# Optimization experiments

Hardware: AMD Instinct MI355X
Metric: run time of the kernel (lower is better)

The kernel has to match this reference:

```python
import jax, jax.numpy as jnp
import numpy as np

MAX_OBJECTS = 20
NODE_DIM = 16
HIDDEN = 64
N_OPS = 8
N_COLORS = 10
B = 65536


def _lin(x, w, b):
    # torch nn.Linear: w is [out, in]
    return x @ w.T + b


def _ln(x, g, b, eps=1e-5):
    mu = x.mean(-1, keepdims=True)
    var = ((x - mu) ** 2).mean(-1, keepdims=True)
    return (x - mu) / jnp.sqrt(var + eps) * g + b


def setup_inputs() -> dict:
    key = jax.random.key(0)
    ks = jax.random.split(key, 32)
    s = 0.1
    d = {
        'node_feats': jax.random.normal(ks[0], (B, MAX_OBJECTS, NODE_DIM), jnp.float32),
        'n_nodes': jax.random.randint(ks[1], (B,), 1, MAX_OBJECTS + 1).astype(jnp.int32),
        'rnn_state': jax.random.normal(ks[2], (B, HIDDEN), jnp.float32),
        'prev_op_onehot': jnp.zeros((B, N_OPS), jnp.float32),
        'ne_w': jax.random.normal(ks[3], (HIDDEN, NODE_DIM)) * s,
        'ne_b': jnp.zeros((HIDDEN,)),
        'mp1_w1': jax.random.normal(ks[4], (HIDDEN, 2 * HIDDEN)) * s,
        'mp1_b1': jnp.zeros((HIDDEN,)),
        'mp1_w2': jax.random.normal(ks[5], (HIDDEN, HIDDEN)) * s,
        'mp1_b2': jnp.zeros((HIDDEN,)),
        'n1_g': jnp.ones((HIDDEN,)),
        'n1_b': jnp.zeros((HIDDEN,)),
        'mp2_w1': jax.random.normal(ks[6], (HIDDEN, 2 * HIDDEN)) * s,
        'mp2_b1': jnp.zeros((HIDDEN,)),
        'mp2_w2': jax.random.normal(ks[7], (HIDDEN, HIDDEN)) * s,
        'mp2_b2': jnp.zeros((HIDDEN,)),
        'n2_g': jnp.ones((HIDDEN,)),
        'n2_b': jnp.zeros((HIDDEN,)),
        'gru_wih': jax.random.normal(ks[8], (3 * HIDDEN, HIDDEN + N_OPS)) * s,
        'gru_whh': jax.random.normal(ks[9], (3 * HIDDEN, HIDDEN)) * s,
        'gru_bih': jnp.zeros((3 * HIDDEN,)),
        'gru_bhh': jnp.zeros((3 * HIDDEN,)),
        'op_w': jax.random.normal(ks[10], (N_OPS, HIDDEN)) * s,
        'op_b': jnp.zeros((N_OPS,)),
        'c1_w': jax.random.normal(ks[11], (N_COLORS, HIDDEN)) * s,
        'c1_b': jnp.zeros((N_COLORS,)),
        'c2_w': jax.random.normal(ks[12], (N_COLORS, HIDDEN)) * s,
        'c2_b': jnp.zeros((N_COLORS,)),
        'pq_w': jax.random.normal(ks[13], (HIDDEN, HIDDEN)) * s,
        'pq_b': jnp.zeros((HIDDEN,)),
        'pk_w': jax.random.normal(ks[14], (HIDDEN, HIDDEN)) * s,
        'pk_b': jnp.zeros((HIDDEN,)),
    }
    return d


def _forward(node_feats, n_nodes, rnn_state, prev_op_onehot,
             ne_w, ne_b, mp1_w1, mp1_b1, mp1_w2, mp1_b2, n1_g, n1_b,
             mp2_w1, mp2_b1, mp2_w2, mp2_b2, n2_g, n2_b,
             gru_wih, gru_whh, gru_bih, gru_bhh,
             op_w, op_b, c1_w, c1_b, c2_w, c2_b, pq_w, pq_b, pk_w, pk_b):
    # ---- encode_graph ----
    h = _lin(node_feats, ne_w, ne_b)                                   # [B, N, H]
    mask = jnp.arange(MAX_OBJECTS)[None, :] < n_nodes[:, None]         # [B, N]
    mf = mask.astype(h.dtype)[..., None]                               # [B, N, 1]
    cnt = jnp.clip(mf.sum(1, keepdims=True), 1.0)                      # [B, 1, 1]
    msg = (h * mf).sum(1, keepdims=True) / cnt                         # [B, 1, H]
    x1 = jnp.concatenate([h, jnp.broadcast_to(msg, h.shape)], -1)
    h = h + _lin(jax.nn.relu(_lin(x1, mp1_w1, mp1_b1)), mp1_w2, mp1_b2)
    h = _ln(h, n1_g, n1_b) * mf
    msg = (h * mf).sum(1, keepdims=True) / cnt
    x2 = jnp.concatenate([h, jnp.broadcast_to(msg, h.shape)], -1)
    h = h + _lin(jax.nn.relu(_lin(x2, mp2_w1, mp2_b1)), mp2_w2, mp2_b2)
    h = _ln(h, n2_g, n2_b) * mf
    graph_vec = (h * mf).sum(1) / jnp.clip(mf.sum(1), 1.0)             # [B, H]
    # ---- step (GRUCell + heads + pointer) ----
    x = jnp.concatenate([graph_vec, prev_op_onehot], -1)               # [B, H+n_ops]
    gi = x @ gru_wih.T + gru_bih                                       # [B, 3H]
    gh = rnn_state @ gru_whh.T + gru_bhh                               # [B, 3H]
    H = HIDDEN
    r = jax.nn.sigmoid(gi[:, :H] + gh[:, :H])
    z = jax.nn.sigmoid(gi[:, H:2 * H] + gh[:, H:2 * H])
    n = jnp.tanh(gi[:, 2 * H:] + r * gh[:, 2 * H:])
    new_state = (1.0 - z) * n + z * rnn_state                          # [B, H]
    op_logits = _lin(new_state, op_w, op_b)
    c1_logits = _lin(new_state, c1_w, c1_b)
    c2_logits = _lin(new_state, c2_w, c2_b)
    query = _lin(new_state, pq_w, pq_b)[:, None, :]                    # [B, 1, H]
    keys = _lin(h, pk_w, pk_b)                                         # [B, N, H]
    ptr_logits = (query * keys).sum(-1)                                # [B, N]
    ptr_logits = jnp.where(mask, ptr_logits, jnp.asarray(-1e9, ptr_logits.dtype))
    return op_logits, c1_logits, c2_logits, ptr_logits, new_state


def reference(node_feats, n_nodes, rnn_state, prev_op_onehot,
              ne_w, ne_b, mp1_w1, mp1_b1, mp1_w2, mp1_b2, n1_g, n1_b,
              mp2_w1, mp2_b1, mp2_w2, mp2_b2, n2_g, n2_b,
              gru_wih, gru_whh, gru_bih, gru_bhh,
              op_w, op_b, c1_w, c1_b, c2_w, c2_b, pq_w, pq_b, pk_w, pk_b):
    return _forward(node_feats, n_nodes, rnn_state, prev_op_onehot,
                    ne_w, ne_b, mp1_w1, mp1_b1, mp1_w2, mp1_b2, n1_g, n1_b,
                    mp2_w1, mp2_b1, mp2_w2, mp2_b2, n2_g, n2_b,
                    gru_wih, gru_whh, gru_bih, gru_bhh,
                    op_w, op_b, c1_w, c1_b, c2_w, c2_b, pq_w, pq_b, pk_w, pk_b)
```

## Files before the change

kernel.cpp:

```cpp
#include <hip/hip_runtime.h>
#include <hip/hip_bf16.h>
#include <cstdint>

#define NM 20
#define NBIN 20
#define MAXB 65536

typedef __attribute__((ext_vector_type(8))) short bf16x8;
typedef __attribute__((ext_vector_type(4))) float f32x4;
typedef __attribute__((ext_vector_type(4))) unsigned int u32x4;

union FU { bf16x8 h; u32x4 u; };

#define MFMA(A, Bf, C) __builtin_amdgcn_mfma_f32_16x16x32_bf16((A), (Bf), (C), 0, 0, 0)

#define F_NE    0
#define F_M1W1  2048
#define F_M1W2  10240
#define F_M2W1  14336
#define F_M2W2  22528
#define F_WIH   26624
#define F_WHH   45056
#define F_PQ    57344
#define F_PK    61440
#define F_PACK  65536
#define F_BNE   67584
#define F_B11   67648
#define F_B12   67712
#define F_G1    67776
#define F_L1    67840
#define F_B21   67904
#define F_B22   67968
#define F_G2    68032
#define F_L2    68096
#define F_TOTAL 68160

__device__ __align__(16) short g_fr[F_TOTAL];
__device__ __align__(16) float g_grb[4][64];
__device__ int g_hist[NBIN];
__device__ int g_off[NBIN];
__device__ int g_done;
__device__ int g_perm[MAXB];

__device__ __forceinline__ short bf16rn(float x) {
  unsigned u = __float_as_uint(x);
  u += 0x7fffu + ((u >> 16) & 1u);
  return (short)(u >> 16);
}
__device__ __forceinline__ float bf2f(short s) {
  return __uint_as_float(((unsigned)(unsigned short)s) << 16);
}
__device__ __forceinline__ unsigned pk2(float lo, float hi) {
  __hip_bfloat162 t = __float22bfloat162_rn(float2{lo, hi});
  return *reinterpret_cast<unsigned*>(&t);
}
__device__ __forceinline__ float fsig(float x) {
  return __builtin_amdgcn_rcpf(1.f + __expf(-x));
}
__device__ __forceinline__ float ftanh(float x) {
  return 1.f - 2.f * __builtin_amdgcn_rcpf(1.f + __expf(2.f * x));
}
__device__ __forceinline__ int s64(int r) {
  int mb = r >> 4, qq = (r >> 2) & 3, i = r & 3;
  return (mb >> 1) * 32 + qq * 8 + (mb & 1) * 4 + i;
}

#define LDF(off) (*(const bf16x8*)(g_fr + (off) + lane * 8))
#define LDB(off, c) (*(const bf16x8*)(g_fr + (off) + (c) * 32 + q * 8))
#define GAF(off) (*(const bf16x8*)(gA + (off)))
#define GBF(off, c) (*(const bf16x8*)(gB + (off) + (c) * 32))

#define BUILDA(OFS, MB, KC, ROWX, GET)                                 \
  for (int idx = t; idx < (MB) * (KC) * 512; idx += T) {               \
    int j = idx & 7, ln = (idx >> 3) & 63, f = idx >> 9;               \
    int mb = f / (KC), kc = f % (KC);                                  \
    int m = mb * 16 + (ln & 15);                                       \
    int k = kc * 32 + (ln >> 4) * 8 + j;                               \
    int row = (ROWX);                                                  \
    (void)row; (void)k; (void)m;                                       \
    g_fr[(OFS) + idx] = bf16rn(GET);                                   \
  }

__global__ void __launch_bounds__(256)
prep_frag(const float* __restrict__ ne_w,
          const float* __restrict__ m1w1, const float* __restrict__ m1w2,
          const float* __restrict__ m2w1, const float* __restrict__ m2w2,
          const float* __restrict__ wih,  const float* __restrict__ whh,
          const float* __restrict__ pqw,  const float* __restrict__ opw,
          const float* __restrict__ c1w,  const float* __restrict__ c2w,
          const float* __restrict__ pkw,
          const float* __restrict__ ne_b,
          const float* __restrict__ m1b1, const float* __restrict__ m1b2,
          const float* __restrict__ n1g,  const float* __restrict__ n1b,
          const float* __restrict__ m2b1, const float* __restrict__ m2b2,
          const float* __restrict__ n2g,  const float* __restrict__ n2b,
          const float* __restrict__ bih,  const float* __restrict__ bhh)
{
  const int t = blockIdx.x * blockDim.x + threadIdx.x;
  const int T = gridDim.x * blockDim.x;
  if (blockIdx.x == 0 && threadIdx.x < NBIN) g_hist[threadIdx.x] = 0;
  if (blockIdx.x == 0 && threadIdx.x == 0) g_done = 0;
  BUILDA(F_NE,   4, 1, s64(m), (k < 16 ? ne_w[row * 16 + k] : (k == 16 ? ne_b[row] : 0.f)))
  BUILDA(F_M1W1, 4, 4, s64(m), m1w1[row * 128 + k])
  BUILDA(F_M1W2, 4, 2, s64(m), m1w2[row * 64 + k])
  BUILDA(F_M2W1, 4, 4, s64(m), m2w1[row * 128 + k])
  BUILDA(F_M2W2, 4, 2, s64(m), m2w2[row * 64 + k])
  BUILDA(F_WIH, 12, 3, (m & 0xC0) | s64(m & 63), (k < 72 ? wih[row * 72 + k] : 0.f))
  BUILDA(F_WHH, 12, 2, (m & 0xC0) | s64(m & 63), whh[row * 64 + k])
  BUILDA(F_PQ,   4, 2, m, pqw[row * 64 + k])
  BUILDA(F_PK,   4, 2, m, pkw[row * 64 + k])
  BUILDA(F_PACK, 2, 2, m, (row < 8 ? opw[row * 64 + k]
                           : row < 18 ? c1w[(row - 8) * 64 + k]
                           : row < 28 ? c2w[(row - 18) * 64 + k] : 0.f))
  for (int i = t; i < 64; i += T) {
    g_fr[F_BNE + i] = bf16rn(ne_b[i]);
    g_fr[F_B11 + i] = bf16rn(m1b1[i]);
    g_fr[F_B12 + i] = bf16rn(m1b2[i]);
    g_fr[F_G1  + i] = bf16rn(n1g[i]);
    g_fr[F_L1  + i] = bf16rn(n1b[i]);
    g_fr[F_B21 + i] = bf16rn(m2b1[i]);
    g_fr[F_B22 + i] = bf16rn(m2b2[i]);
    g_fr[F_G2  + i] = bf16rn(n2g[i]);
    g_fr[F_L2  + i] = bf16rn(n2b[i]);
    g_grb[0][i] = bih[i]       + bhh[i];
    g_grb[1][i] = bih[64 + i]  + bhh[64 + i];
    g_grb[2][i] = bih[128 + i];
    g_grb[3][i] = bhh[128 + i];
  }
}

__global__ void __launch_bounds__(256)
nn_hist(const int* __restrict__ nnp, int B)
{
  __shared__ int lh[NBIN];
  __shared__ int lastdone;
  const int t = threadIdx.x;
  if (t < NBIN) lh[t] = 0;
  __syncthreads();
  for (int i = blockIdx.x * blockDim.x + t; i < B; i += gridDim.x * blockDim.x)
    atomicAdd(&lh[nnp[i] - 1], 1);
  __syncthreads();
  if (t < NBIN && lh[t] > 0) atomicAdd(&g_hist[t], lh[t]);
  __threadfence();
  if (t == 0) lastdone = (atomicAdd(&g_done, 1) == (int)gridDim.x - 1);
  __syncthreads();
  if (t == 0 && lastdone) {
    int acc = 0;
    for (int i = NBIN - 1; i >= 0; i--) { g_off[i] = acc; acc += g_hist[i]; }
  }
}

__global__ void __launch_bounds__(256)
nn_scatter(const int* __restrict__ nnp, int B)
{
  __shared__ int lc[NBIN], lbase[NBIN];
  const int t = threadIdx.x;
  const int i = blockIdx.x * 256 + t;
  if (t < NBIN) lc[t] = 0;
  __syncthreads();
  int bin = 0, r = 0;
  const bool ok = (i < B);
  if (ok) { bin = nnp[i] - 1; r = atomicAdd(&lc[bin], 1); }
  __syncthreads();
  if (t < NBIN) lbase[t] = (lc[t] > 0) ? atomicAdd(&g_off[t], lc[t]) : 0;
  __syncthreads();
  if (ok) g_perm[lbase[bin] + r] = i;
}

__device__ __forceinline__ void pack8(FU& f, const float* v) {
  f.u[0] = pk2(v[0], v[1]); f.u[1] = pk2(v[2], v[3]);
  f.u[2] = pk2(v[4], v[5]); f.u[3] = pk2(v[6], v[7]);
}

__device__ __forceinline__ void mp_stage(
    FU hA[][2], const FU* msgf,
    int w1off, int w2off, int b1o, int b2o, int lgo, int lbo,
    int nnv, int wv, int nact, int lane, int q)
{
  if (nact == 0) return;
  const f32x4 zf4 = {0.f, 0.f, 0.f, 0.f};
  f32x4 tmsg[4];
  #pragma unroll
  for (int mb = 0; mb < 4; mb++) {
    tmsg[mb] = MFMA(LDF(w1off + (mb * 4 + 2) * 512), msgf[0].h, zf4);
    tmsg[mb] = MFMA(LDF(w1off + (mb * 4 + 3) * 512), msgf[1].h, tmsg[mb]);
  }
  {
    FU b1p0, b1p1; b1p0.h = LDB(b1o, 0); b1p1.h = LDB(b1o, 1);
    #pragma unroll
    for (int mb = 0; mb < 4; mb++)
      #pragma unroll
      for (int i = 0; i < 4; i++)
        tmsg[mb][i] += bf2f(((mb >> 1) ? b1p1 : b1p0).h[(mb & 1) * 4 + i]);
  }

  #pragma unroll
  for (int t = 0; t < 5; t++) {
    if (t < nact) {
      int tz = 0;
      asm volatile("" : "+v"(tz));
      const short* gA = g_fr + lane * 8 + tz;
      const short* gB = g_fr + q * 8 + tz;
      const int n = wv + 4 * t;
      f32x4 T[4];
      #pragma unroll
      for (int mb = 0; mb < 4; mb++) {
        T[mb] = MFMA(GAF(w1off + (mb * 4 + 0) * 512), hA[t][0].h, tmsg[mb]);
        T[mb] = MFMA(GAF(w1off + (mb * 4 + 1) * 512), hA[t][1].h, T[mb]);
      }
      FU tb[2];
      #pragma unroll
      for (int c = 0; c < 2; c++)
        #pragma unroll
        for (int w = 0; w < 4; w++) {
          int mb = 2 * c + (w >> 1), i0 = (w & 1) * 2;
          float lo = fmaxf(T[mb][i0],     0.f);
          float hi = fmaxf(T[mb][i0 + 1], 0.f);
          tb[c].u[w] = pk2(lo, hi);
        }
      f32x4 H[4];
      #pragma unroll
      for (int mb = 0; mb < 4; mb++) {
        H[mb] = MFMA(GAF(w2off + (mb * 2 + 0) * 512), tb[0].h, zf4);
        H[mb] = MFMA(GAF(w2off + (mb * 2 + 1) * 512), tb[1].h, H[mb]);
      }
      FU b2p0, b2p1;
      b2p0.h = GBF(b2o, 0); b2p1.h = GBF(b2o, 1);
      float y[16]; float s = 0.f, ss = 0.f;
      #pragma unroll
      for (int k = 0; k < 16; k++) {
        int c = k >> 3, j = k & 7;
        float v = H[2 * c + (j >> 2)][j & 3] + bf2f((c ? b2p1 : b2p0).h[j]) +
                  bf2f(hA[t][c].h[j]);
        y[k] = v; s += v; ss += v * v;
      }
      s += __shfl_xor(s, 16, 64); ss += __shfl_xor(ss, 16, 64);
      s += __shfl_xor(s, 32, 64); ss += __shfl_xor(ss, 32, 64);
      float mu = s * 0.015625f;
      float rstd = rsqrtf(ss * 0.015625f - mu * mu + 1e-5f);
      float mfv = (n < nnv) ? 1.f : 0.f;
      FU lgp0, lgp1, lbp0, lbp1;
      lgp0.h = GBF(lgo, 0); lgp1.h = GBF(lgo, 1);
      lbp0.h = GBF(lbo, 0); lbp1.h = GBF(lbo, 1);
      #pragma unroll
      for (int k = 0; k < 16; k++) {
        int c = k >> 3, j = k & 7;
        float hv = ((y[k] - mu) * rstd * bf2f((c ? lgp1 : lgp0).h[j]) +
                    bf2f((c ? lbp1 : lbp0).h[j])) * mfv;
        y[k] = hv;
      }
      pack8(hA[t][0], y); pack8(hA[t][1], y + 8);
    }
  }
}

__global__ void __launch_bounds__(256)
msp(const float* __restrict__ nf, const int* __restrict__ nnp,
    const float* __restrict__ rnn, const float* __restrict__ poh,
    const float* __restrict__ opb, const float* __restrict__ c1b,
    const float* __restrict__ c2b, const float* __restrict__ pqb,
    const float* __restrict__ pkb,
    float* __restrict__ out, int B)
{
  __shared__ __align__(16) float exch[2][4][64][17];
  __shared__ __align__(16) unsigned nsx[64][8];

  const int tid = threadIdx.x;
  const int wv = tid >> 6;
  const int lane = tid & 63;
  const int l15 = lane & 15, q = lane >> 4;
  const int b0 = blockIdx.x * 16;
  const int bb = g_perm[b0 + l15];

  const int nnv = nnp[bb];
  const float inv = 1.0f / (float)nnv;
  const f32x4 zf4 = {0.f, 0.f, 0.f, 0.f};

  int M = nnv;
  { int o;
    o = __shfl_xor(M, 1, 64); M = M > o ? M : o;
    o = __shfl_xor(M, 2, 64); M = M > o ? M : o;
    o = __shfl_xor(M, 4, 64); M = M > o ? M : o;
    o = __shfl_xor(M, 8, 64); M = M > o ? M : o; }
  int nact = (M - wv + 3) >> 2;
  nact = nact < 0 ? 0 : (nact > 5 ? 5 : nact);

  FU hA[5][2];

  {
    float4 xa[5][2];
    #pragma unroll
    for (int t = 0; t < 5; t++) {
      if (t < nact && q < 2) {
        const float* p = nf + ((size_t)bb * NM + (wv + 4 * t)) * 16 + q * 8;
        xa[t][0] = *(const float4*)p;
        xa[t][1] = *(const float4*)(p + 4);
      }
    }
    #pragma unroll
    for (int t = 0; t < 5; t++) {
      if (t < nact) {
        int tz = 0;
        asm volatile("" : "+v"(tz));
        const short* gA = g_fr + lane * 8 + tz;
        const int n = wv + 4 * t;
        FU bx;
        bx.u[0] = 0; bx.u[1] = 0; bx.u[2] = 0; bx.u[3] = 0;
        if (q < 2) {
          bx.u[0] = pk2(xa[t][0].x, xa[t][0].y); bx.u[1] = pk2(xa[t][0].z, xa[t][0].w);
          bx.u[2] = pk2(xa[t][1].x, xa[t][1].y); bx.u[3] = pk2(xa[t][1].z, xa[t][1].w);
        } else if (q == 2) {
          bx.u[0] = pk2(1.f, 0.f);
        }
        f32x4 C[4];
        #pragma unroll
        for (int mb = 0; mb < 4; mb++) C[mb] = MFMA(GAF(F_NE + mb * 512), bx.h, zf4);
        const float mfv = (n < nnv) ? 1.f : 0.f;
        float hv[16];
        #pragma unroll
        for (int k = 0; k < 16; k++) {
          int c = k >> 3, j = k & 7;
          hv[k] = C[2 * c + (j >> 2)][j & 3] * mfv;
        }
        pack8(hA[t][0], hv); pack8(hA[t][1], hv + 8);
      }
    }
    #pragma unroll
    for (int t = 0; t < 5; t++) {
      if (t >= nact) {
        #pragma unroll
        for (int c = 0; c < 2; c++) {
          hA[t][c].u[0] = 0; hA[t][c].u[1] = 0;
          hA[t][c].u[2] = 0; hA[t][c].u[3] = 0;
        }
      }
    }
  }

  FU msgf[2];
  #define EXCHANGE(REG)                                                        \
    {                                                                          \
      _Pragma("unroll")                                                        \
      for (int k = 0; k < 16; k++) {                                           \
        int c = k >> 3, j = k & 7;                                             \
        float sK = bf2f(hA[0][c].h[j]) + bf2f(hA[1][c].h[j]) +                 \
                   bf2f(hA[2][c].h[j]) + bf2f(hA[3][c].h[j]) +                 \
                   bf2f(hA[4][c].h[j]);                                        \
        exch[REG][wv][lane][k] = sK;                                           \
      }                                                                        \
      __syncthreads();                                                         \
      _Pragma("unroll")                                                        \
      for (int w8 = 0; w8 < 8; w8++) {                                         \
        int k0 = 2 * w8, k1 = k0 + 1;                                          \
        float a = (exch[REG][0][lane][k0] + exch[REG][1][lane][k0] +           \
                   exch[REG][2][lane][k0] + exch[REG][3][lane][k0]) * inv;     \
        float b = (exch[REG][0][lane][k1] + exch[REG][1][lane][k1] +           \
                   exch[REG][2][lane][k1] + exch[REG][3][lane][k1]) * inv;     \
        FU* dp = (w8 < 4) ? &msgf[0] : &msgf[1];                               \
        dp->u[w8 & 3] = pk2(a, b);                                             \
      }                                                                        \
    }

  EXCHANGE(0)
  mp_stage(hA, msgf, F_M1W1, F_M1W2, F_B11, F_B12, F_G1, F_L1, nnv, wv, nact, lane, q);

  EXCHANGE(1)
  mp_stage(hA, msgf, F_M2W1, F_M2W2, F_B21, F_B22, F_G2, F_L2, nnv, wv, nact, lane, q);

  EXCHANGE(0)

  {
    FU px;
    if (q == 0) {
      const float* pp = poh + (size_t)bb * 8;
      float4 p0 = *(const float4*)pp, p1 = *(const float4*)(pp + 4);
      px.u[0] = pk2(p0.x, p0.y); px.u[1] = pk2(p0.z, p0.w);
      px.u[2] = pk2(p1.x, p1.y); px.u[3] = pk2(p1.z, p1.w);
    } else { px.u[0] = 0; px.u[1] = 0; px.u[2] = 0; px.u[3] = 0; }
    const float* rr0 = rnn + (size_t)bb * 64;
    float rv[16];
    #pragma unroll
    for (int c = 0; c < 2; c++) {
      float4 a0 = *(const float4*)(rr0 + c * 32 + q * 8);
      float4 a1 = *(const float4*)(rr0 + c * 32 + q * 8 + 4);
      rv[c * 8 + 0] = a0.x; rv[c * 8 + 1] = a0.y; rv[c * 8 + 2] = a0.z; rv[c * 8 + 3] = a0.w;
      rv[c * 8 + 4] = a1.x; rv[c * 8 + 5] = a1.y; rv[c * 8 + 6] = a1.z; rv[c * 8 + 7] = a1.w;
    }
    FU ah[2]; pack8(ah[0], rv); pack8(ah[1], rv + 8);

    const int tt = wv;
    f32x4 R = MFMA(LDF(F_WIH + (tt * 3 + 0) * 512), msgf[0].h, zf4);
    R = MFMA(LDF(F_WIH + (tt * 3 + 1) * 512), msgf[1].h, R);
    R = MFMA(LDF(F_WIH + (tt * 3 + 2) * 512), px.h, R);
    R = MFMA(LDF(F_WHH + (tt * 2 + 0) * 512), ah[0].h, R);
    R = MFMA(LDF(F_WHH + (tt * 2 + 1) * 512), ah[1].h, R);
    f32x4 Z = MFMA(LDF(F_WIH + ((4 + tt) * 3 + 0) * 512), msgf[0].h, zf4);
    Z = MFMA(LDF(F_WIH + ((4 + tt) * 3 + 1) * 512), msgf[1].h, Z);
    Z = MFMA(LDF(F_WIH + ((4 + tt) * 3 + 2) * 512), px.h, Z);
    Z = MFMA(LDF(F_WHH + ((4 + tt) * 2 + 0) * 512), ah[0].h, Z);
    Z = MFMA(LDF(F_WHH + ((4 + tt) * 2 + 1) * 512), ah[1].h, Z);
    f32x4 Ni = MFMA(LDF(F_WIH + ((8 + tt) * 3 + 0) * 512), msgf[0].h, zf4);
    Ni = MFMA(LDF(F_WIH + ((8 + tt) * 3 + 1) * 512), msgf[1].h, Ni);
    Ni = MFMA(LDF(F_WIH + ((8 + tt) * 3 + 2) * 512), px.h, Ni);
    f32x4 Nh = MFMA(LDF(F_WHH + ((8 + tt) * 2 + 0) * 512), ah[0].h, zf4);
    Nh = MFMA(LDF(F_WHH + ((8 + tt) * 2 + 1) * 512), ah[1].h, Nh);

    const int dbase = q * 8 + (tt >> 1) * 32 + (tt & 1) * 4;
    f32x4 brv = *(const f32x4*)&g_grb[0][dbase];
    f32x4 bzv = *(const f32x4*)&g_grb[1][dbase];
    f32x4 bnv = *(const f32x4*)&g_grb[2][dbase];
    f32x4 bhv = *(const f32x4*)&g_grb[3][dbase];
    float nsv[4];
    #pragma unroll
    for (int i = 0; i < 4; i++) {
      const int K = (tt >> 1) * 32 + (tt & 1) * 4 + i;
      const int d = q * 8 + K;
      float rr = fsig(R[i] + brv[i]);
      float zz = fsig(Z[i] + bzv[i]);
      float ng = ftanh(Ni[i] + bnv[i] + rr * (Nh[i] + bhv[i]));
      float st = rv[(tt >> 1) * 8 + (tt & 1) * 4 + i];
      float v = (1.f - zz) * ng + zz * st;
      out[(size_t)B * 48 + (size_t)bb * 64 + d] = v;
      nsv[i] = v;
    }
    const int dw = (tt >> 1) * 4 + (tt & 1) * 2;
    nsx[lane][dw]     = pk2(nsv[0], nsv[1]);
    nsx[lane][dw + 1] = pk2(nsv[2], nsv[3]);
  }
  __syncthreads();

  {
    FU an0, an1;
    an0.u = *(const u32x4*)&nsx[lane][0];
    an1.u = *(const u32x4*)&nsx[lane][4];
    float qv[16];
    #pragma unroll
    for (int mb = 0; mb < 4; mb++) {
      f32x4 Qc = MFMA(LDF(F_PQ + (mb * 2 + 0) * 512), an0.h, zf4);
      Qc = MFMA(LDF(F_PQ + (mb * 2 + 1) * 512), an1.h, Qc);
      f32x4 pq4 = *(const f32x4*)&pqb[mb * 16 + q * 4];
      #pragma unroll
      for (int i = 0; i < 4; i++) qv[mb * 4 + i] = Qc[i] + pq4[i];
    }
    float qb = 0.f;
    #pragma unroll
    for (int mb = 0; mb < 4; mb++) {
      f32x4 pk4 = *(const f32x4*)&pkb[mb * 16 + q * 4];
      #pragma unroll
      for (int i = 0; i < 4; i++) qb += qv[mb * 4 + i] * pk4[i];
    }
    qb += __shfl_xor(qb, 16, 64); qb += __shfl_xor(qb, 32, 64);

    if (wv < 2) {
      f32x4 L = MFMA(LDF(F_PACK + (wv * 2 + 0) * 512), an0.h, zf4);
      L = MFMA(LDF(F_PACK + (wv * 2 + 1) * 512), an1.h, L);
      #pragma unroll
      for (int i = 0; i < 4; i++) {
        int o = wv * 16 + q * 4 + i;
        if (o < 8)       out[(size_t)bb * 8 + o] = L[i] + opb[o];
        else if (o < 18) out[(size_t)B * 8 + (size_t)bb * 10 + (o - 8)] = L[i] + c1b[o - 8];
        else if (o < 28) out[(size_t)B * 18 + (size_t)bb * 10 + (o - 18)] = L[i] + c2b[o - 18];
      }
    }
    #pragma unroll
    for (int t = 0; t < 5; t++) {
      const int n = wv + 4 * t;
      if (t < nact) {
        int tz = 0;
        asm volatile("" : "+v"(tz));
        const short* gA = g_fr + lane * 8 + tz;
        float dt = 0.f;
        #pragma unroll
        for (int mb = 0; mb < 4; mb++) {
          f32x4 Kc = MFMA(GAF(F_PK + (mb * 2 + 0) * 512), hA[t][0].h, zf4);
          Kc = MFMA(GAF(F_PK + (mb * 2 + 1) * 512), hA[t][1].h, Kc);
          #pragma unroll
          for (int i = 0; i < 4; i++) dt += qv[mb * 4 + i] * Kc[i];
        }
        dt += __shfl_xor(dt, 16, 64); dt += __shfl_xor(dt, 32, 64);
        if (q == 0)
          out[(size_t)B * 28 + (size_t)bb * 20 + n] = (n < nnv) ? (dt + qb) : -1e9f;
      } else {
        if (q == 0)
          out[(size_t)B * 28 + (size_t)bb * 20 + n] = -1e9f;
      }
    }
  }
}

extern "C" void kernel_launch(void* const* d_in, const int* in_sizes, int n_in,
                              void* d_out, int out_size, void* d_ws, size_t ws_size,
                              hipStream_t stream)
{
  (void)n_in; (void)out_size; (void)d_ws; (void)ws_size;
  const float* nf   = (const float*)d_in[0];
  const int*   nnp  = (const int*)  d_in[1];
  const float* rnn  = (const float*)d_in[2];
  const float* poh  = (const float*)d_in[3];
  const float* ne_w = (const float*)d_in[4];
  const float* ne_b = (const float*)d_in[5];
  const float* m1w1 = (const float*)d_in[6];
  const float* m1b1 = (const float*)d_in[7];
  const float* m1w2 = (const float*)d_in[8];
  const float* m1b2 = (const float*)d_in[9];
  const float* n1g  = (const float*)d_in[10];
  const float* n1b  = (const float*)d_in[11];
  const float* m2w1 = (const float*)d_in[12];
  const float* m2b1 = (const float*)d_in[13];
  const float* m2w2 = (const float*)d_in[14];
  const float* m2b2 = (const float*)d_in[15];
  const float* n2g  = (const float*)d_in[16];
  const float* n2b  = (const float*)d_in[17];
  const float* wih  = (const float*)d_in[18];
  const float* whh  = (const float*)d_in[19];
  const float* bih  = (const float*)d_in[20];
  const float* bhh  = (const float*)d_in[21];
  const float* opw  = (const float*)d_in[22];
  const float* opb  = (const float*)d_in[23];
  const float* c1w  = (const float*)d_in[24];
  const float* c1b  = (const float*)d_in[25];
  const float* c2w  = (const float*)d_in[26];
  const float* c2b  = (const float*)d_in[27];
  const float* pqw  = (const float*)d_in[28];
  const float* pqb  = (const float*)d_in[29];
  const float* pkw  = (const float*)d_in[30];
  const float* pkb  = (const float*)d_in[31];
  float* out = (float*)d_out;
  const int B = in_sizes[1];

  prep_frag<<<132, 256, 0, stream>>>(ne_w, m1w1, m1w2, m2w1, m2w2,
                                     wih, whh, pqw, opw, c1w, c2w, pkw,
                                     ne_b, m1b1, m1b2, n1g, n1b,
                                     m2b1, m2b2, n2g, n2b, bih, bhh);
  nn_hist<<<256, 256, 0, stream>>>(nnp, B);
  nn_scatter<<<(B + 255) / 256, 256, 0, stream>>>(nnp, B);
  msp<<<B / 16, 256, 0, stream>>>(nf, nnp, rnn, poh,
                                  opb, c1b, c2b,
                                  pqb, pkb, out, B);
}
```

Measured before the change: 401.8 us.

## Fuse histogram into prep kernel, accumulate node sums in registers, double-buffer loads

```diff
diff --git a/kernel.cpp b/kernel.cpp
--- a/kernel.cpp
+++ b/kernel.cpp
@@ -94,12 +94,11 @@
           const float* __restrict__ n1g,  const float* __restrict__ n1b,
           const float* __restrict__ m2b1, const float* __restrict__ m2b2,
           const float* __restrict__ n2g,  const float* __restrict__ n2b,
-          const float* __restrict__ bih,  const float* __restrict__ bhh)
+          const float* __restrict__ bih,  const float* __restrict__ bhh,
+          const int* __restrict__ nnp, int B)
 {
   const int t = blockIdx.x * blockDim.x + threadIdx.x;
   const int T = gridDim.x * blockDim.x;
-  if (blockIdx.x == 0 && threadIdx.x < NBIN) g_hist[threadIdx.x] = 0;
-  if (blockIdx.x == 0 && threadIdx.x == 0) g_done = 0;
   BUILDA(F_NE,   4, 1, s64(m), (k < 16 ? ne_w[row * 16 + k] : (k == 16 ? ne_b[row] : 0.f)))
   BUILDA(F_M1W1, 4, 4, s64(m), m1w1[row * 128 + k])
   BUILDA(F_M1W2, 4, 2, s64(m), m1w2[row * 64 + k])
@@ -127,26 +126,25 @@
     g_grb[2][i] = bih[128 + i];
     g_grb[3][i] = bhh[128 + i];
   }
-}
-
-__global__ void __launch_bounds__(256)
-nn_hist(const int* __restrict__ nnp, int B)
-{
+
   __shared__ int lh[NBIN];
   __shared__ int lastdone;
-  const int t = threadIdx.x;
-  if (t < NBIN) lh[t] = 0;
-  __syncthreads();
-  for (int i = blockIdx.x * blockDim.x + t; i < B; i += gridDim.x * blockDim.x)
-    atomicAdd(&lh[nnp[i] - 1], 1);
-  __syncthreads();
-  if (t < NBIN && lh[t] > 0) atomicAdd(&g_hist[t], lh[t]);
+  const int lt = threadIdx.x;
+  if (lt < NBIN) lh[lt] = 0;
+  __syncthreads();
+  for (int i = t; i < B; i += T) atomicAdd(&lh[nnp[i] - 1], 1);
+  __syncthreads();
+  if (lt < NBIN && lh[lt] > 0) atomicAdd(&g_hist[lt], lh[lt]);
   __threadfence();
-  if (t == 0) lastdone = (atomicAdd(&g_done, 1) == (int)gridDim.x - 1);
-  __syncthreads();
-  if (t == 0 && lastdone) {
+  if (lt == 0) lastdone = (atomicAdd(&g_done, 1) == (int)gridDim.x - 1);
+  __syncthreads();
+  if (lastdone && lt == 0) {
+    __threadfence();
     int acc = 0;
-    for (int i = NBIN - 1; i >= 0; i--) { g_off[i] = acc; acc += g_hist[i]; }
+    for (int i = NBIN - 1; i >= 0; i--) {
+      g_off[i] = acc; acc += g_hist[i]; g_hist[i] = 0;
+    }
+    g_done = 0;
   }
 }
 
@@ -173,7 +171,7 @@
 }
 
 __device__ __forceinline__ void mp_stage(
-    FU hA[][2], const FU* msgf,
+    FU hA[][2], float* macc, const FU* msgf,
     int w1off, int w2off, int b1o, int b2o, int lgo, int lbo,
     int nnv, int wv, int nact, int lane, int q)
 {
@@ -247,7 +245,7 @@
         int c = k >> 3, j = k & 7;
         float hv = ((y[k] - mu) * rstd * bf2f((c ? lgp1 : lgp0).h[j]) +
                     bf2f((c ? lbp1 : lbp0).h[j])) * mfv;
-        y[k] = hv;
+        macc[k] += hv; y[k] = hv;
       }
       pack8(hA[t][0], y); pack8(hA[t][1], y + 8);
     }
@@ -286,20 +284,27 @@
   nact = nact < 0 ? 0 : (nact > 5 ? 5 : nact);
 
   FU hA[5][2];
+  float mac[16];
+  #pragma unroll
+  for (int k = 0; k < 16; k++) mac[k] = 0.f;
 
   {
-    float4 xa[5][2];
-    #pragma unroll
-    for (int t = 0; t < 5; t++) {
-      if (t < nact && q < 2) {
-        const float* p = nf + ((size_t)bb * NM + (wv + 4 * t)) * 16 + q * 8;
-        xa[t][0] = *(const float4*)p;
-        xa[t][1] = *(const float4*)(p + 4);
-      }
+    float4 xaA[2], xaB[2];
+    if (nact > 0 && q < 2) {
+      const float* p = nf + ((size_t)bb * NM + wv) * 16 + q * 8;
+      xaA[0] = *(const float4*)p; xaA[1] = *(const float4*)(p + 4);
     }
     #pragma unroll
     for (int t = 0; t < 5; t++) {
       if (t < nact) {
+        float4 c0, c1;
+        if ((t & 1) == 0) { c0 = xaA[0]; c1 = xaA[1]; }
+        else              { c0 = xaB[0]; c1 = xaB[1]; }
+        if (t + 1 < nact && q < 2) {
+          const float* p = nf + ((size_t)bb * NM + (wv + 4 * (t + 1))) * 16 + q * 8;
+          if ((t & 1) == 0) { xaB[0] = *(const float4*)p; xaB[1] = *(const float4*)(p + 4); }
+          else              { xaA[0] = *(const float4*)p; xaA[1] = *(const float4*)(p + 4); }
+        }
         int tz = 0;
         asm volatile("" : "+v"(tz));
         const short* gA = g_fr + lane * 8 + tz;
@@ -307,8 +312,8 @@
         FU bx;
         bx.u[0] = 0; bx.u[1] = 0; bx.u[2] = 0; bx.u[3] = 0;
         if (q < 2) {
-          bx.u[0] = pk2(xa[t][0].x, xa[t][0].y); bx.u[1] = pk2(xa[t][0].z, xa[t][0].w);
-          bx.u[2] = pk2(xa[t][1].x, xa[t][1].y); bx.u[3] = pk2(xa[t][1].z, xa[t][1].w);
+          bx.u[0] = pk2(c0.x, c0.y); bx.u[1] = pk2(c0.z, c0.w);
+          bx.u[2] = pk2(c1.x, c1.y); bx.u[3] = pk2(c1.z, c1.w);
         } else if (q == 2) {
           bx.u[0] = pk2(1.f, 0.f);
         }
@@ -321,18 +326,9 @@
         for (int k = 0; k < 16; k++) {
           int c = k >> 3, j = k & 7;
           hv[k] = C[2 * c + (j >> 2)][j & 3] * mfv;
+          mac[k] += hv[k];
         }
         pack8(hA[t][0], hv); pack8(hA[t][1], hv + 8);
-      }
-    }
-    #pragma unroll
-    for (int t = 0; t < 5; t++) {
-      if (t >= nact) {
-        #pragma unroll
-        for (int c = 0; c < 2; c++) {
-          hA[t][c].u[0] = 0; hA[t][c].u[1] = 0;
-          hA[t][c].u[2] = 0; hA[t][c].u[3] = 0;
-        }
       }
     }
   }
@@ -341,13 +337,7 @@
   #define EXCHANGE(REG)                                                        \
     {                                                                          \
       _Pragma("unroll")                                                        \
-      for (int k = 0; k < 16; k++) {                                           \
-        int c = k >> 3, j = k & 7;                                             \
-        float sK = bf2f(hA[0][c].h[j]) + bf2f(hA[1][c].h[j]) +                 \
-                   bf2f(hA[2][c].h[j]) + bf2f(hA[3][c].h[j]) +                 \
-                   bf2f(hA[4][c].h[j]);                                        \
-        exch[REG][wv][lane][k] = sK;                                           \
-      }                                                                        \
+      for (int k = 0; k < 16; k++) exch[REG][wv][lane][k] = mac[k];            \
       __syncthreads();                                                         \
       _Pragma("unroll")                                                        \
       for (int w8 = 0; w8 < 8; w8++) {                                         \
@@ -359,13 +349,15 @@
         FU* dp = (w8 < 4) ? &msgf[0] : &msgf[1];                               \
         dp->u[w8 & 3] = pk2(a, b);                                             \
       }                                                                        \
+      _Pragma("unroll")                                                        \
+      for (int k = 0; k < 16; k++) mac[k] = 0.f;                               \
     }
 
   EXCHANGE(0)
-  mp_stage(hA, msgf, F_M1W1, F_M1W2, F_B11, F_B12, F_G1, F_L1, nnv, wv, nact, lane, q);
+  mp_stage(hA, mac, msgf, F_M1W1, F_M1W2, F_B11, F_B12, F_G1, F_L1, nnv, wv, nact, lane, q);
 
   EXCHANGE(1)
-  mp_stage(hA, msgf, F_M2W1, F_M2W2, F_B21, F_B22, F_G2, F_L2, nnv, wv, nact, lane, q);
+  mp_stage(hA, mac, msgf, F_M2W1, F_M2W2, F_B21, F_B22, F_G2, F_L2, nnv, wv, nact, lane, q);
 
   EXCHANGE(0)
 
@@ -462,18 +454,21 @@
         else if (o < 28) out[(size_t)B * 18 + (size_t)bb * 10 + (o - 18)] = L[i] + c2b[o - 18];
       }
     }
+    bf16x8 pkA[4][2];
+    #pragma unroll
+    for (int mb = 0; mb < 4; mb++) {
+      pkA[mb][0] = LDF(F_PK + (mb * 2 + 0) * 512);
+      pkA[mb][1] = LDF(F_PK + (mb * 2 + 1) * 512);
+    }
     #pragma unroll
     for (int t = 0; t < 5; t++) {
       const int n = wv + 4 * t;
       if (t < nact) {
-        int tz = 0;
-        asm volatile("" : "+v"(tz));
-        const short* gA = g_fr + lane * 8 + tz;
         float dt = 0.f;
         #pragma unroll
         for (int mb = 0; mb < 4; mb++) {
-          f32x4 Kc = MFMA(GAF(F_PK + (mb * 2 + 0) * 512), hA[t][0].h, zf4);
-          Kc = MFMA(GAF(F_PK + (mb * 2 + 1) * 512), hA[t][1].h, Kc);
+          f32x4 Kc = MFMA(pkA[mb][0], hA[t][0].h, zf4);
+          Kc = MFMA(pkA[mb][1], hA[t][1].h, Kc);
           #pragma unroll
           for (int i = 0; i < 4; i++) dt += qv[mb * 4 + i] * Kc[i];
         }
@@ -531,8 +526,8 @@
   prep_frag<<<132, 256, 0, stream>>>(ne_w, m1w1, m1w2, m2w1, m2w2,
                                      wih, whh, pqw, opw, c1w, c2w, pkw,
                                      ne_b, m1b1, m1b2, n1g, n1b,
-                                     m2b1, m2b2, n2g, n2b, bih, bhh);
-  nn_hist<<<256, 256, 0, stream>>>(nnp, B);
+                                     m2b1, m2b2, n2g, n2b, bih, bhh,
+                                     nnp, B);
   nn_scatter<<<(B + 255) / 256, 256, 0, stream>>>(nnp, B);
   msp<<<B / 16, 256, 0, stream>>>(nf, nnp, rnn, poh,
                                   opb, c1b, c2b,
```

Measured after the change: 390.4 us. 2.8% less time.
